# Kernel tuning notes

Measured on AMD Instinct MI355X. Metric: run time of the kernel, lower is better.

Reference implementation:

```python
import jax, jax.numpy as jnp
import numpy as np

LAM = 0.1
E = float(np.e)


def _lambertw0(y, iters=8):
    """Principal branch W0(y) for y >= -1/e via series init + Halley iterations.

    Matches scipy.special.lambertw(y).real on the real principal branch.
    """
    # Series expansion around the branch point y = -1/e (w = -1):
    #   w ~= -1 + p - p^2/3 + (11/72) p^3,  p = sqrt(2 (e*y + 1))
    p = jnp.sqrt(jnp.maximum(2.0 * (E * y + 1.0), 0.0))
    w_branch = -1.0 + p - p * p / 3.0 + (11.0 / 72.0) * p ** 3
    w = jnp.where(y < 0.0, w_branch, jnp.log1p(y))
    for _ in range(iters):
        ew = jnp.exp(w)
        f = w * ew - y
        wp1 = w + 1.0
        safe_wp1 = jnp.where(jnp.abs(wp1) < 1e-6, 1e-6, wp1)
        denom = ew * wp1 - (w + 2.0) * f / (2.0 * safe_wp1)
        denom = jnp.where(jnp.abs(denom) < 1e-12, 1e-12, denom)
        w = w - f / denom
    return w


def setup_inputs() -> dict:
    key = jax.random.key(0)
    N = 33_554_432  # 2^25 per-sample losses, ~128 MB fp32
    loss = jax.random.uniform(key, (N,), dtype=jnp.float32)
    return {"loss": loss}


def reference(loss):
    # First call: counter 0 -> 1, so tau = mean(detach(loss)).
    l_i = jax.lax.stop_gradient(loss)
    tau = jnp.mean(l_i)
    # sigma(l_i): y = 0.5 * max(-2/e, (l_i - tau)/lam); sigma = exp(-W0(y))
    y = 0.5 * jnp.maximum(jnp.float32(-2.0 / E), (l_i - tau) / LAM)
    sigma = jnp.exp(-_lambertw0(y))  # stop-graded (built from l_i)
    out = (loss - tau) * sigma + LAM * jnp.log(sigma) ** 2
    return out
```

## Files before the change

### kernel.cpp

```cpp
#include <hip/hip_runtime.h>
#include <math.h>


#define NPART 2048
#define E_F 2.7182818f
#define NEG_INV_E (-0.36787942f)

__device__ __forceinline__ float fast_rcp(float x) {
    return __builtin_amdgcn_rcpf(x);
}

__device__ __forceinline__ float superloss_elem(float l, float tau) {
    float d = l - tau;
    float t5 = 5.0f * d;
    float y = fmaxf(NEG_INV_E, t5);
    float ey1 = fmaf(E_F, y, 1.0f);
    float p2 = fmaxf(ey1 + ey1, 0.0f);
    float p = __builtin_amdgcn_sqrtf(p2);
    float num = fmaf(p, fmaf(p, 0.018055f, 0.5f), 1.0f);
    float den = fmaf(p, fmaf(p, 0.143051f, 0.833323f), 1.0f);
    float wp1 = p * num * fast_rcp(den);
    float w = wp1 - 1.0f;
    float ew = __expf(w);
    float f = fmaf(w, ew, -y);
    float den2 = fmaf(ew, wp1, 1e-4f);
    w = fmaf(-f, fast_rcp(den2), w);
    float out_u = 0.1f * (w * (w + 2.0f));
    float out_c = fmaf(E_F, d, 0.1f);
    return (t5 < NEG_INV_E) ? out_c : out_u;
}

__global__ void reduce_partial(const float4* __restrict__ x, float* __restrict__ partials,
                               int n4, const float* __restrict__ x_scalar, int n) {
    float s = 0.0f;
    int stride = gridDim.x * blockDim.x;
    for (int i = blockIdx.x * blockDim.x + threadIdx.x; i < n4; i += stride) {
        float4 v = x[i];
        s += (v.x + v.y) + (v.z + v.w);
    }
    if (blockIdx.x == 0 && threadIdx.x == 0) {
        for (int i = 4 * n4; i < n; ++i) s += x_scalar[i];
    }
#pragma unroll
    for (int off = 32; off > 0; off >>= 1) s += __shfl_down(s, off, 64);
    __shared__ float smem[4];
    int lane = threadIdx.x & 63;
    int wave = threadIdx.x >> 6;
    if (lane == 0) smem[wave] = s;
    __syncthreads();
    if (threadIdx.x == 0) {
        partials[blockIdx.x] = (smem[0] + smem[1]) + (smem[2] + smem[3]);
    }
}

__global__ void finalize_tau(const float* __restrict__ partials, float* __restrict__ tau_p, int n) {
    double s = 0.0;
    for (int i = threadIdx.x; i < NPART; i += 256) s += (double)partials[i];
#pragma unroll
    for (int off = 32; off > 0; off >>= 1) s += __shfl_down(s, off, 64);
    __shared__ double smem[4];
    int lane = threadIdx.x & 63;
    int wave = threadIdx.x >> 6;
    if (lane == 0) smem[wave] = s;
    __syncthreads();
    if (threadIdx.x == 0) {
        double total = (smem[0] + smem[1]) + (smem[2] + smem[3]);
        tau_p[0] = (float)(total / (double)n);
    }
}

__global__ void superloss_main(const float4* __restrict__ x, float4* __restrict__ out,
                               const float* __restrict__ tau_p, int n4) {
    int i = blockIdx.x * blockDim.x + threadIdx.x;
    if (i >= n4) return;
    float tau = *tau_p;
    float4 v = x[i];
    float4 r;
    r.x = superloss_elem(v.x, tau);
    r.y = superloss_elem(v.y, tau);
    r.z = superloss_elem(v.z, tau);
    r.w = superloss_elem(v.w, tau);
    out[i] = r;
}

__global__ void superloss_tail(const float* __restrict__ x, float* __restrict__ out,
                               const float* __restrict__ tau_p, int start, int n) {
    int i = start + blockIdx.x * blockDim.x + threadIdx.x;
    if (i < n) out[i] = superloss_elem(x[i], *tau_p);
}

extern "C" void kernel_launch(void* const* d_in, const int* in_sizes, int n_in,
                              void* d_out, int out_size, void* d_ws, size_t ws_size,
                              hipStream_t stream) {
    const float* loss = (const float*)d_in[0];
    float* out = (float*)d_out;
    int n = in_sizes[0];
    int n4 = n / 4;
    float* ws = (float*)d_ws;
    float* tau_p = ws + NPART;

    reduce_partial<<<NPART, 256, 0, stream>>>((const float4*)loss, ws, n4, loss, n);
    finalize_tau<<<1, 256, 0, stream>>>(ws, tau_p, n);

    int blocks = (n4 + 255) / 256;
    superloss_main<<<blocks, 256, 0, stream>>>((const float4*)loss, (float4*)out, tau_p, n4);

    int tail = n - 4 * n4;
    if (tail > 0) {
        superloss_tail<<<(tail + 255) / 256, 256, 0, stream>>>(loss, out, tau_p, 4 * n4, n);
    }
}
```

Baseline: 243.9 us.

## Fuse reduction and elementwise pass into one cooperative kernel with grid sync

Replaces the four-launch sequence (partial reduce, finalize, main, tail) with a single cooperative kernel that reduces, grid-syncs, has each block recompute tau from the partials, then runs the elementwise loop. This removes the inter-kernel launch gaps and the serial single-block finalize step. In exchange it adds grid-sync cost, redundant per-block summation of partials, and a persistent grid-stride loop whose occupancy comes from a runtime query, with the old path kept as a fallback.

```diff
diff --git a/kernel.cpp b/kernel.cpp
--- a/kernel.cpp
+++ b/kernel.cpp
@@ -1,7 +1,12 @@
 #include <hip/hip_runtime.h>
+#include <hip/hip_cooperative_groups.h>
 #include <math.h>
 
-
+namespace cg = cooperative_groups;
+
+
+#define TPB 256
+#define MAXBLOCKS 2048
 #define NPART 2048
 #define E_F 2.7182818f
 #define NEG_INV_E (-0.36787942f)
@@ -30,6 +35,67 @@
     return (t5 < NEG_INV_E) ? out_c : out_u;
 }
 
+
+__global__ __launch_bounds__(TPB) void superloss_fused(
+    const float4* __restrict__ x, float4* __restrict__ out,
+    float* __restrict__ ws,
+    const float* __restrict__ x_s, float* __restrict__ out_s,
+    int n4, int n, int nblocks)
+{
+    const int tid = blockIdx.x * TPB + threadIdx.x;
+    const int stride = nblocks * TPB;
+    const int lane = threadIdx.x & 63;
+    const int wv = threadIdx.x >> 6;
+
+    float s = 0.0f;
+    for (int i = tid; i < n4; i += stride) {
+        float4 v = x[i];
+        s += (v.x + v.y) + (v.z + v.w);
+    }
+    if (blockIdx.x == 0 && threadIdx.x == 0) {
+        for (int i = 4 * n4; i < n; ++i) s += x_s[i];
+    }
+#pragma unroll
+    for (int off = 32; off > 0; off >>= 1) s += __shfl_down(s, off, 64);
+    __shared__ float smem[4];
+    if (lane == 0) smem[wv] = s;
+    __syncthreads();
+    if (threadIdx.x == 0) {
+        ws[blockIdx.x] = (smem[0] + smem[1]) + (smem[2] + smem[3]);
+    }
+
+    cg::this_grid().sync();
+
+    double dacc = 0.0;
+    for (int i = threadIdx.x; i < nblocks; i += TPB) dacc += (double)ws[i];
+#pragma unroll
+    for (int off = 32; off > 0; off >>= 1) dacc += __shfl_down(dacc, off, 64);
+    __shared__ double dsm[4];
+    if (lane == 0) dsm[wv] = dacc;
+    __syncthreads();
+    __shared__ float tau_sh;
+    if (threadIdx.x == 0) {
+        double total = (dsm[0] + dsm[1]) + (dsm[2] + dsm[3]);
+        tau_sh = (float)(total / (double)n);
+    }
+    __syncthreads();
+    const float tau = tau_sh;
+
+    for (int i = tid; i < n4; i += stride) {
+        float4 v = x[i];
+        float4 r;
+        r.x = superloss_elem(v.x, tau);
+        r.y = superloss_elem(v.y, tau);
+        r.z = superloss_elem(v.z, tau);
+        r.w = superloss_elem(v.w, tau);
+        out[i] = r;
+    }
+    for (int i = 4 * n4 + tid; i < n; i += stride) {
+        out_s[i] = superloss_elem(x_s[i], tau);
+    }
+}
+
+
 __global__ void reduce_partial(const float4* __restrict__ x, float* __restrict__ partials,
                                int n4, const float* __restrict__ x_scalar, int n) {
     float s = 0.0f;
@@ -97,16 +163,38 @@
     int n = in_sizes[0];
     int n4 = n / 4;
     float* ws = (float*)d_ws;
-    float* tau_p = ws + NPART;
-
-    reduce_partial<<<NPART, 256, 0, stream>>>((const float4*)loss, ws, n4, loss, n);
-    finalize_tau<<<1, 256, 0, stream>>>(ws, tau_p, n);
-
-    int blocks = (n4 + 255) / 256;
-    superloss_main<<<blocks, 256, 0, stream>>>((const float4*)loss, (float4*)out, tau_p, n4);
-
-    int tail = n - 4 * n4;
-    if (tail > 0) {
-        superloss_tail<<<(tail + 255) / 256, 256, 0, stream>>>(loss, out, tau_p, 4 * n4, n);
-    }
-}
+
+    static int coop_blocks = -1;
+    if (coop_blocks < 0) {
+        int nb = 0;
+        hipError_t e = hipOccupancyMaxActiveBlocksPerMultiprocessor(
+            &nb, (const void*)superloss_fused, TPB, 0);
+        if (e != hipSuccess || nb < 1) nb = 4;
+        long b = (long)nb * 256;
+        if (b > MAXBLOCKS) b = MAXBLOCKS;
+        if (b < 256) b = 256;
+        coop_blocks = (int)b;
+    }
+
+    const float4* x4 = (const float4*)loss;
+    float4* o4 = (float4*)out;
+    const float* xs = loss;
+    float* os = out;
+    int nb_ = coop_blocks;
+    void* args[] = {(void*)&x4, (void*)&o4, (void*)&ws, (void*)&xs, (void*)&os,
+                    (void*)&n4, (void*)&n, (void*)&nb_};
+    hipError_t err = hipLaunchCooperativeKernel((const void*)superloss_fused,
+                                                dim3(coop_blocks), dim3(TPB),
+                                                args, 0, stream);
+    if (err != hipSuccess) {
+        float* tau_p = ws + NPART;
+        reduce_partial<<<NPART, 256, 0, stream>>>((const float4*)loss, ws, n4, loss, n);
+        finalize_tau<<<1, 256, 0, stream>>>(ws, tau_p, n);
+        int blocks = (n4 + 255) / 256;
+        superloss_main<<<blocks, 256, 0, stream>>>((const float4*)loss, (float4*)out, tau_p, n4);
+        int tail = n - 4 * n4;
+        if (tail > 0) {
+            superloss_tail<<<(tail + 255) / 256, 256, 0, stream>>>(loss, out, tau_p, 4 * n4, n);
+        }
+    }
+}
```

After: 333.8 us. 1.37x slower.
